# Optimization experiments

Hardware: AMD Instinct MI355X
Metric: run time of the kernel (lower is better)

Reference implementation:

```python
import jax, jax.numpy as jnp
import numpy as np


def setup_inputs() -> dict:
    key = jax.random.key(0)
    kx, k1, k2 = jax.random.split(key, 3)
    x = jax.random.normal(kx, (2, 1, 256, 256), dtype=jnp.float32)
    # keras 'random_normal' initializer: stddev=0.05
    w1 = jax.random.normal(k1, (1,), dtype=jnp.float32) * 0.05
    w2 = jax.random.normal(k2, (1,), dtype=jnp.float32) * 0.05
    return {"x": x, "w1": w1, "w2": w2}


def reference(x, w1, w2):
    # x: [B, 1, H, W] (channels_first, single channel as implied by kernel in_ch=1)
    # SAME padding (TF: pad_left = (k-1)//2 = (i+1)//2). Each conv is equivalent to
    #   y_i[w] = w1 * x[w - (i+1)//2] + w2 * x[w + (i+2)//2]   (zero outside [0, W))
    # Outputs are concatenated on axis=1 -> [B, W, H, W].
    B, C, H, W = x.shape
    x2 = x[:, 0]  # [B, H, W]
    i = jnp.arange(W)[:, None]   # shift index -> output channel
    w = jnp.arange(W)[None, :]   # spatial position
    idx1 = w - (i + 1) // 2      # [W_i, W_w]
    idx2 = w + (i + 2) // 2      # [W_i, W_w]
    m1 = ((idx1 >= 0) & (idx1 < W)).astype(x.dtype)
    m2 = ((idx2 >= 0) & (idx2 < W)).astype(x.dtype)
    g1 = jnp.take(x2, jnp.clip(idx1, 0, W - 1), axis=2)  # [B, H, W_i, W_w]
    g2 = jnp.take(x2, jnp.clip(idx2, 0, W - 1), axis=2)  # [B, H, W_i, W_w]
    out = w1[0] * g1 * m1 + w2[0] * g2 * m2
    return jnp.transpose(out, (0, 2, 1, 3))  # [B, W_i, H, W_w]
```

## Files before the change

### kernel.cpp

```cpp
#include <hip/hip_runtime.h>


__global__ __launch_bounds__(256) void ConvolutionalOverlap_kernel(
    const float* __restrict__ x,
    const float* __restrict__ w1p,
    const float* __restrict__ w2p,
    float* __restrict__ out)
{
    __shared__ float lds[512];

    const int bid = blockIdx.x;
    const int b   = bid >> 10;
    const int h   = (bid >> 2) & 255;
    const int ic  = bid & 3;
    const int t   = threadIdx.x;

    if (t < 128) lds[t] = 0.0f;
    else         lds[256 + t] = 0.0f;
    lds[128 + t] = x[(b << 16) + (h << 8) + t];
    __syncthreads();

    const float w1 = w1p[0];
    const float w2 = w2p[0];

    const int lane = t & 63;
    const int wv   = t >> 6;
    const int w0   = lane << 2;

    #pragma unroll 4
    for (int it = 0; it < 16; ++it) {
        const int i  = (ic << 6) + (it << 2) + wv;
        const int s1 = (i + 1) >> 1;
        const int s2 = (i + 2) >> 1;

        const int a1 = 128 - s1 + w0;
        const int a2 = 128 + s2 + w0;

        float4 o;
        o.x = w1 * lds[a1]     + w2 * lds[a2];
        o.y = w1 * lds[a1 + 1] + w2 * lds[a2 + 1];
        o.z = w1 * lds[a1 + 2] + w2 * lds[a2 + 2];
        o.w = w1 * lds[a1 + 3] + w2 * lds[a2 + 3];

        float4* dst = reinterpret_cast<float4*>(
            out + (b << 24) + (i << 16) + (h << 8) + w0);
        *dst = o;
    }
}

extern "C" void kernel_launch(void* const* d_in, const int* in_sizes, int n_in,
                              void* d_out, int out_size, void* d_ws, size_t ws_size,
                              hipStream_t stream) {
    const float* x  = (const float*)d_in[0];
    const float* w1 = (const float*)d_in[1];
    const float* w2 = (const float*)d_in[2];
    float* out = (float*)d_out;

    const int grid  = 2 * 256 * 4;
    const int block = 256;

    hipLaunchKernelGGL(ConvolutionalOverlap_kernel, dim3(grid), dim3(block), 0,
                       stream, x, w1, w2, out);
}
```

Baseline: 156.5 us.

## Drop LDS staging, read row directly, use scalar nontemporal stores

Each thread now reads its two input elements straight from global memory, served by cache, instead of staging the row in shared memory behind a barrier. Each thread handles one output column across 64 channels and writes one float with a nontemporal store, where before it wrote float4 vectors. The goal is to remove the LDS fill and the sync and to keep the large output write stream from polluting the cache. The risk is that scalar stores issue four times as many store instructions, and repeated global loads may cost more than LDS reads.

New measurement: 144.4 us. 7.7% less time.

```diff
diff --git a/kernel.cpp b/kernel.cpp
--- a/kernel.cpp
+++ b/kernel.cpp
@@ -7,44 +7,34 @@
     const float* __restrict__ w2p,
     float* __restrict__ out)
 {
-    __shared__ float lds[512];
-
+    const int t   = threadIdx.x;
     const int bid = blockIdx.x;
     const int b   = bid >> 10;
     const int h   = (bid >> 2) & 255;
     const int ic  = bid & 3;
-    const int t   = threadIdx.x;
-
-    if (t < 128) lds[t] = 0.0f;
-    else         lds[256 + t] = 0.0f;
-    lds[128 + t] = x[(b << 16) + (h << 8) + t];
-    __syncthreads();
 
     const float w1 = w1p[0];
     const float w2 = w2p[0];
 
-    const int lane = t & 63;
-    const int wv   = t >> 6;
-    const int w0   = lane << 2;
+    const float* __restrict__ row = x + (b << 16) + (h << 8);
+    float* __restrict__ op = out + (b << 24) + (ic << 22) + (h << 8) + t;
 
-    #pragma unroll 4
-    for (int it = 0; it < 16; ++it) {
-        const int i  = (ic << 6) + (it << 2) + wv;
+    #pragma unroll 8
+    for (int ii = 0; ii < 64; ++ii) {
+        const int i  = (ic << 6) + ii;
         const int s1 = (i + 1) >> 1;
         const int s2 = (i + 2) >> 1;
 
-        const int a1 = 128 - s1 + w0;
-        const int a2 = 128 + s2 + w0;
+        const int a1 = t - s1;
+        const int a2 = t + s2;
 
-        float4 o;
-        o.x = w1 * lds[a1]     + w2 * lds[a2];
-        o.y = w1 * lds[a1 + 1] + w2 * lds[a2 + 1];
-        o.z = w1 * lds[a1 + 2] + w2 * lds[a2 + 2];
-        o.w = w1 * lds[a1 + 3] + w2 * lds[a2 + 3];
+        float v1 = row[a1 < 0 ? 0 : a1];
+        float v2 = row[a2 > 255 ? 255 : a2];
+        v1 = (a1 < 0)   ? 0.0f : v1;
+        v2 = (a2 > 255) ? 0.0f : v2;
 
-        float4* dst = reinterpret_cast<float4*>(
-            out + (b << 24) + (i << 16) + (h << 8) + w0);
-        *dst = o;
+        __builtin_nontemporal_store(w1 * v1 + w2 * v2, op);
+        op += 1 << 16;
     }
 }
 
@@ -56,9 +46,6 @@
     const float* w2 = (const float*)d_in[2];
     float* out = (float*)d_out;
 
-    const int grid  = 2 * 256 * 4;
-    const int block = 256;
-
-    hipLaunchKernelGGL(ConvolutionalOverlap_kernel, dim3(grid), dim3(block), 0,
+    hipLaunchKernelGGL(ConvolutionalOverlap_kernel, dim3(2048), dim3(256), 0,
                        stream, x, w1, w2, out);
 }
```
